# Kernel optimization log

Measured on AMD Instinct MI355X. Metric: run time of the kernel, lower is better.

The kernel has to match this reference:

```python
import jax, jax.numpy as jnp
import numpy as np

B, L, D = 4, 512, 128

def setup_inputs() -> dict:
    key = jax.random.key(0)
    k1, k2, k3, k4 = jax.random.split(key, 4)
    s = 1.0 / np.sqrt(D)
    return {
        "inp": jax.random.normal(k1, (B, L, D), dtype=jnp.float32),
        "Wu": jax.random.normal(k2, (D, D), dtype=jnp.float32) * s,
        "Ww": jax.random.normal(k3, (D, D), dtype=jnp.float32) * s,
        "Wv": jax.random.normal(k4, (1, D), dtype=jnp.float32) * s,
    }

def reference(inp, Wu, Ww, Wv):
    # inp: (B,L,D); torch Linear weights are (out,in), so y = x @ W.T
    qu = inp @ Wu.T                      # (B,L,D), u(inp)
    kw = inp @ Ww.T                      # (B,L,D), w(inp)
    # qu.unsqueeze(1) -> broadcast over i; kw.unsqueeze(2) -> broadcast over j
    # h[b,i,j,:] = tanh(u(inp)[b,j] + w(inp)[b,i])   (dropout = identity in eval)
    h = jnp.tanh(qu[:, None, :, :] + kw[:, :, None, :])   # (B,L,L,D)
    score = jnp.einsum('bijd,d->bij', h, Wv[0])           # (B,L,L)
    attn = jax.nn.softmax(score, axis=2)                  # softmax over keys j
    out = jnp.einsum('bij,bjd->bid', attn, inp)           # bmm(attn, inp)
    return out, attn
```

## Files before the change

kernel.cpp:

```cpp
#include <hip/hip_runtime.h>

#define BD 128
#define SL 512
#define NB 4

__device__ __forceinline__ float rcp_fast(float x) { return __builtin_amdgcn_rcpf(x); }

__global__ __launch_bounds__(256) void k_tr(const float* __restrict__ Wu,
                                            const float* __restrict__ Ww,
                                            float* __restrict__ WuT,
                                            float* __restrict__ WwT) {
    int idx = blockIdx.x * 256 + threadIdx.x;
    int k = idx >> 7, o = idx & 127;
    WuT[idx] = Wu[o * BD + k];
    WwT[idx] = Ww[o * BD + k];
}

__global__ __launch_bounds__(256) void k_qk(const float* __restrict__ inp,
                                            const float* __restrict__ WuT,
                                            const float* __restrict__ WwT,
                                            float* __restrict__ Equ,
                                            float* __restrict__ Ekw) {
    __shared__ float sx[2][BD];
    const int t = threadIdx.x, m = t >> 7, o = t & 127;
    const int blk = blockIdx.x;
    const int x   = blk & 7;
    const int b   = x >> 1;
    const int rp  = (blk >> 3) * 2 + (x & 1);
    const int r0  = b * SL + rp * 2;
    const int l0  = rp * 2;

    sx[t >> 7][t & 127] = inp[(size_t)r0 * BD + t];
    __syncthreads();

    const float* WT = m ? WwT : WuT;
    float acc0 = 0.f, acc1 = 0.f;
    #pragma unroll 4
    for (int k = 0; k < BD; k += 4) {
        float w0 = WT[(k + 0) * BD + o];
        float w1 = WT[(k + 1) * BD + o];
        float w2 = WT[(k + 2) * BD + o];
        float w3 = WT[(k + 3) * BD + o];
        float4 x0 = *(const float4*)&sx[0][k];
        float4 x1 = *(const float4*)&sx[1][k];
        acc0 = fmaf(x0.x, w0, acc0); acc0 = fmaf(x0.y, w1, acc0);
        acc0 = fmaf(x0.z, w2, acc0); acc0 = fmaf(x0.w, w3, acc0);
        acc1 = fmaf(x1.x, w0, acc1); acc1 = fmaf(x1.y, w1, acc1);
        acc1 = fmaf(x1.z, w2, acc1); acc1 = fmaf(x1.w, w3, acc1);
    }

    if (m == 0) {
        size_t base = ((size_t)b * 32 + (o >> 2)) * (SL * 4) + (size_t)l0 * 4 + (o & 3);
        Equ[base]     = __expf(2.f * acc0);
        Equ[base + 4] = __expf(2.f * acc1);
    } else {
        Ekw[(size_t)(r0 + 0) * BD + o] = __expf(2.f * acc0);
        Ekw[(size_t)(r0 + 1) * BD + o] = __expf(2.f * acc1);
    }
}

__device__ __forceinline__ void quad_acc(const float4 q, const float4 u4,
                                         const float4 e, float& acc) {
    float x0 = fmaf(q.x, e.x, u4.x);
    float x1 = fmaf(q.y, e.y, u4.y);
    float x2 = fmaf(q.z, e.z, u4.z);
    float x3 = fmaf(q.w, e.w, u4.w);
    float p01 = x0 * x1, p23 = x2 * x3;
    float num = fmaf(x0 + x1, p23, (x2 + x3) * p01);
    acc = fmaf(num, rcp_fast(p01 * p23), acc);
}

__global__ __launch_bounds__(512, 4) void k_attn(const float* __restrict__ inp,
                                                 const float* __restrict__ Wv,
                                                 const float* __restrict__ Equ,
                                                 const float* __restrict__ Ekw,
                                                 float* __restrict__ out,
                                                 float* __restrict__ attn) {
    __shared__ float4 s_E2[32][4];
    __shared__ float4 s_u4[32];
    __shared__ float4 s_pT[SL];
    __shared__ float  s_fin[32 * BD];
    __shared__ float4 s_red[8];

    const int j   = threadIdx.x;
    const int blk = blockIdx.x;
    const int x   = blk & 7;
    const int b   = x >> 1;
    const int it  = (blk >> 3) * 2 + (x & 1);
    const int i0  = it * 4;

    if (j < BD) {
        const float* ek = Ekw + ((size_t)b * SL + i0) * BD + j;
        float u = rcp_fast(Wv[j]);
        int c = j >> 2, kk = j & 3;
        ((float*)&s_E2[c][0])[kk] = ek[0]        * u;
        ((float*)&s_E2[c][1])[kk] = ek[BD]       * u;
        ((float*)&s_E2[c][2])[kk] = ek[2 * BD]   * u;
        ((float*)&s_E2[c][3])[kk] = ek[3 * BD]   * u;
        ((float*)&s_u4[c])[kk]    = u;
    }
    __syncthreads();

    const float4* equ4 = (const float4*)(Equ) + (size_t)b * 32 * SL;
    float a0 = 0.f, a1 = 0.f, a2 = 0.f, a3 = 0.f;
    #pragma unroll 4
    for (int c = 0; c < 32; ++c) {
        float4 q  = equ4[c * SL + j];
        float4 u4 = s_u4[c];
        float4 e0 = s_E2[c][0];
        float4 e1 = s_E2[c][1];
        float4 e2 = s_E2[c][2];
        float4 e3 = s_E2[c][3];
        quad_acc(q, u4, e0, a0);
        quad_acc(q, u4, e1, a1);
        quad_acc(q, u4, e2, a2);
        quad_acc(q, u4, e3, a3);
    }

    float p0 = __expf(-2.f * a0);
    float p1 = __expf(-2.f * a1);
    float p2 = __expf(-2.f * a2);
    float p3 = __expf(-2.f * a3);
    float r0 = p0, r1 = p1, r2 = p2, r3 = p3;
    #pragma unroll
    for (int off = 32; off > 0; off >>= 1) {
        r0 += __shfl_xor(r0, off, 64);
        r1 += __shfl_xor(r1, off, 64);
        r2 += __shfl_xor(r2, off, 64);
        r3 += __shfl_xor(r3, off, 64);
    }
    const int w = j >> 6, ln = j & 63;
    if (ln == 0) s_red[w] = make_float4(r0, r1, r2, r3);
    __syncthreads();
    float4 d0 = s_red[0], d1 = s_red[1], d2 = s_red[2], d3 = s_red[3];
    float4 d4 = s_red[4], d5 = s_red[5], d6 = s_red[6], d7 = s_red[7];
    float dx = ((d0.x + d1.x) + (d2.x + d3.x)) + ((d4.x + d5.x) + (d6.x + d7.x));
    float dy = ((d0.y + d1.y) + (d2.y + d3.y)) + ((d4.y + d5.y) + (d6.y + d7.y));
    float dz = ((d0.z + d1.z) + (d2.z + d3.z)) + ((d4.z + d5.z) + (d6.z + d7.z));
    float dw = ((d0.w + d1.w) + (d2.w + d3.w)) + ((d4.w + d5.w) + (d6.w + d7.w));
    float n0 = p0 * rcp_fast(dx);
    float n1 = p1 * rcp_fast(dy);
    float n2 = p2 * rcp_fast(dz);
    float n3 = p3 * rcp_fast(dw);
    float* ap = attn + ((size_t)b * SL + i0) * SL + j;
    ap[0]      = n0;
    ap[SL]     = n1;
    ap[2 * SL] = n2;
    ap[3 * SL] = n3;
    s_pT[j] = make_float4(n0, n1, n2, n3);
    __syncthreads();

    const int g  = j >> 6;
    const int dq = j & 31;
    const int rh = (j >> 5) & 1;
    const float4* inp4 = (const float4*)(inp) + (size_t)b * SL * 32;
    float4 accA = make_float4(0.f, 0.f, 0.f, 0.f);
    float4 accB = make_float4(0.f, 0.f, 0.f, 0.f);
    #pragma unroll 4
    for (int tt = 0; tt < 64; ++tt) {
        int jr = g * 64 + tt;
        float4 xv = inp4[jr * 32 + dq];
        float2 pp = *((const float2*)&s_pT[jr] + rh);
        accA.x = fmaf(pp.x, xv.x, accA.x); accA.y = fmaf(pp.x, xv.y, accA.y);
        accA.z = fmaf(pp.x, xv.z, accA.z); accA.w = fmaf(pp.x, xv.w, accA.w);
        accB.x = fmaf(pp.y, xv.x, accB.x); accB.y = fmaf(pp.y, xv.y, accB.y);
        accB.z = fmaf(pp.y, xv.z, accB.z); accB.w = fmaf(pp.y, xv.w, accB.w);
    }
    *(float4*)&s_fin[((g * 4) + rh * 2 + 0) * BD + dq * 4] = accA;
    *(float4*)&s_fin[((g * 4) + rh * 2 + 1) * BD + dq * 4] = accB;
    __syncthreads();
    {
        int row = j >> 7, d = j & 127;
        float s = 0.f;
        #pragma unroll
        for (int gg = 0; gg < 8; ++gg)
            s += s_fin[(gg * 4 + row) * BD + d];
        out[((size_t)b * SL + i0 + row) * BD + d] = s;
    }
}

extern "C" void kernel_launch(void* const* d_in, const int* in_sizes, int n_in,
                              void* d_out, int out_size, void* d_ws, size_t ws_size,
                              hipStream_t stream) {
    const float* inp = (const float*)d_in[0];
    const float* Wu  = (const float*)d_in[1];
    const float* Ww  = (const float*)d_in[2];
    const float* Wv  = (const float*)d_in[3];

    float* out  = (float*)d_out;
    float* attn = out + (size_t)NB * SL * BD;

    float* ws   = (float*)d_ws;
    float* Equ  = ws;
    float* Ekw  = Equ + (size_t)NB * BD * SL;
    float* WuT  = Ekw + (size_t)NB * SL * BD;
    float* WwT  = WuT + BD * BD;

    k_tr  <<<BD * BD / 256, 256, 0, stream>>>(Wu, Ww, WuT, WwT);
    k_qk  <<<NB * SL / 2, 256, 0, stream>>>(inp, WuT, WwT, Equ, Ekw);
    k_attn<<<NB * SL / 4, 512, 0, stream>>>(inp, Wv, Equ, Ekw, out, attn);
}
```

Baseline: 89.77 us.

## Fuse projection and attention into one cooperative kernel with grid sync

```diff
diff --git a/kernel.cpp b/kernel.cpp
--- a/kernel.cpp
+++ b/kernel.cpp
@@ -1,10 +1,217 @@
 #include <hip/hip_runtime.h>
+#include <hip/hip_cooperative_groups.h>
 
 #define BD 128
 #define SL 512
 #define NB 4
 
+namespace cg = cooperative_groups;
+
 __device__ __forceinline__ float rcp_fast(float x) { return __builtin_amdgcn_rcpf(x); }
+
+
+struct QkMem { float x[64][130]; float e[16][65]; };
+struct AtMem {
+    float4 E2[32][4];
+    float4 u4[32];
+    float4 pT[SL];
+    float  fin[32 * BD];
+    float4 red[8];
+};
+
+__global__ __launch_bounds__(512, 4) void k_fused(const float* __restrict__ inp,
+                                                  const float* __restrict__ Wu,
+                                                  const float* __restrict__ Ww,
+                                                  const float* __restrict__ Wv,
+                                                  float* __restrict__ Equ,
+                                                  float* __restrict__ Ekw,
+                                                  float* __restrict__ out,
+                                                  float* __restrict__ attn) {
+    constexpr size_t SM_BYTES = sizeof(QkMem) > sizeof(AtMem) ? sizeof(QkMem) : sizeof(AtMem);
+    __shared__ __align__(16) unsigned char smraw[SM_BYTES];
+    QkMem& qk = *reinterpret_cast<QkMem*>(smraw);
+    AtMem& at = *reinterpret_cast<AtMem*>(smraw);
+
+    const int t   = threadIdx.x;
+    const int blk = blockIdx.x;
+    const int x   = blk & 7;
+    const int b   = x >> 1;
+
+    {
+        const int jb = ((blk >> 3) << 1) | (x & 1);
+        const int m  = jb & 1;
+        const int o0 = ((jb >> 1) & 7) << 4;
+        const int rc = jb >> 4;
+        const int R0 = b * SL + rc * 64;
+
+        #pragma unroll
+        for (int c = 0; c < 16; ++c) {
+            int lin = c * 512 + t;
+            qk.x[lin >> 7][lin & 127] = inp[(size_t)R0 * BD + lin];
+        }
+        __syncthreads();
+
+        const int w = t >> 6, l = t & 63;
+        const int ou = __builtin_amdgcn_readfirstlane(o0 + (w << 1));
+        const float* __restrict__ Wm = m ? Ww : Wu;
+        const float* __restrict__ W0 = Wm + (size_t)ou * BD;
+        const float* __restrict__ W1 = W0 + BD;
+        float acc0 = 0.f, acc1 = 0.f;
+        #pragma unroll 8
+        for (int k = 0; k < BD; k += 2) {
+            float2 xv = *(const float2*)&qk.x[l][k];
+            float wa0 = W0[k], wb0 = W0[k + 1];
+            float wa1 = W1[k], wb1 = W1[k + 1];
+            acc0 = fmaf(xv.x, wa0, acc0); acc0 = fmaf(xv.y, wb0, acc0);
+            acc1 = fmaf(xv.x, wa1, acc1); acc1 = fmaf(xv.y, wb1, acc1);
+        }
+        qk.e[(w << 1) + 0][l] = __expf(2.f * acc0);
+        qk.e[(w << 1) + 1][l] = __expf(2.f * acc1);
+        __syncthreads();
+
+        if (m) {
+            #pragma unroll
+            for (int ph = 0; ph < 2; ++ph) {
+                int e   = ph * 512 + t;
+                int row = e >> 4, ol = e & 15;
+                Ekw[(size_t)(R0 + row) * BD + o0 + ol] = qk.e[ol][row];
+            }
+        } else {
+            float* Eb = Equ + (((size_t)b * 32 + (o0 >> 2)) * SL + rc * 64) * 4;
+            #pragma unroll
+            for (int ph = 0; ph < 2; ++ph) {
+                int e  = ph * 512 + t;
+                int cL = e >> 8, lj = (e >> 2) & 63, kk = e & 3;
+                Eb[((size_t)cL * SL + lj) * 4 + kk] = qk.e[cL * 4 + kk][lj];
+            }
+        }
+    }
+
+    __threadfence();
+    cg::this_grid().sync();
+
+    const int it = ((blk >> 3) << 1) | (x & 1);
+    const int i0 = it * 4;
+    const int j  = t;
+
+    if (j < BD) {
+        const float* ek = Ekw + ((size_t)b * SL + i0) * BD + j;
+        float u = rcp_fast(Wv[j]);
+        int c = j >> 2, kk = j & 3;
+        ((float*)&at.E2[c][0])[kk] = ek[0]      * u;
+        ((float*)&at.E2[c][1])[kk] = ek[BD]     * u;
+        ((float*)&at.E2[c][2])[kk] = ek[2 * BD] * u;
+        ((float*)&at.E2[c][3])[kk] = ek[3 * BD] * u;
+        ((float*)&at.u4[c])[kk]    = u;
+    }
+    __syncthreads();
+
+    const float4* equ4 = (const float4*)(Equ) + (size_t)b * 32 * SL;
+    float a0 = 0.f, a1 = 0.f, a2 = 0.f, a3 = 0.f;
+    #pragma unroll 4
+    for (int c = 0; c < 32; ++c) {
+        float4 q  = equ4[c * SL + j];
+        float4 u4 = at.u4[c];
+        float4 e0 = at.E2[c][0];
+        float4 e1 = at.E2[c][1];
+        float4 e2 = at.E2[c][2];
+        float4 e3 = at.E2[c][3];
+        {
+            float x0 = fmaf(q.x, e0.x, u4.x), x1 = fmaf(q.y, e0.y, u4.y);
+            float x2 = fmaf(q.z, e0.z, u4.z), x3 = fmaf(q.w, e0.w, u4.w);
+            float p01 = x0 * x1, p23 = x2 * x3;
+            float num = fmaf(x0 + x1, p23, (x2 + x3) * p01);
+            a0 = fmaf(num, rcp_fast(p01 * p23), a0);
+        }
+        {
+            float x0 = fmaf(q.x, e1.x, u4.x), x1 = fmaf(q.y, e1.y, u4.y);
+            float x2 = fmaf(q.z, e1.z, u4.z), x3 = fmaf(q.w, e1.w, u4.w);
+            float p01 = x0 * x1, p23 = x2 * x3;
+            float num = fmaf(x0 + x1, p23, (x2 + x3) * p01);
+            a1 = fmaf(num, rcp_fast(p01 * p23), a1);
+        }
+        {
+            float x0 = fmaf(q.x, e2.x, u4.x), x1 = fmaf(q.y, e2.y, u4.y);
+            float x2 = fmaf(q.z, e2.z, u4.z), x3 = fmaf(q.w, e2.w, u4.w);
+            float p01 = x0 * x1, p23 = x2 * x3;
+            float num = fmaf(x0 + x1, p23, (x2 + x3) * p01);
+            a2 = fmaf(num, rcp_fast(p01 * p23), a2);
+        }
+        {
+            float x0 = fmaf(q.x, e3.x, u4.x), x1 = fmaf(q.y, e3.y, u4.y);
+            float x2 = fmaf(q.z, e3.z, u4.z), x3 = fmaf(q.w, e3.w, u4.w);
+            float p01 = x0 * x1, p23 = x2 * x3;
+            float num = fmaf(x0 + x1, p23, (x2 + x3) * p01);
+            a3 = fmaf(num, rcp_fast(p01 * p23), a3);
+        }
+    }
+
+    float p0 = __expf(-2.f * a0);
+    float p1 = __expf(-2.f * a1);
+    float p2 = __expf(-2.f * a2);
+    float p3 = __expf(-2.f * a3);
+    float r0 = p0, r1 = p1, r2 = p2, r3 = p3;
+    #pragma unroll
+    for (int off = 32; off > 0; off >>= 1) {
+        r0 += __shfl_xor(r0, off, 64);
+        r1 += __shfl_xor(r1, off, 64);
+        r2 += __shfl_xor(r2, off, 64);
+        r3 += __shfl_xor(r3, off, 64);
+    }
+    const int wv8 = j >> 6, ln = j & 63;
+    if (ln == 0) at.red[wv8] = make_float4(r0, r1, r2, r3);
+    __syncthreads();
+    {
+        float4 d0 = at.red[0], d1 = at.red[1], d2 = at.red[2], d3 = at.red[3];
+        float4 d4 = at.red[4], d5 = at.red[5], d6 = at.red[6], d7 = at.red[7];
+        float dx = ((d0.x + d1.x) + (d2.x + d3.x)) + ((d4.x + d5.x) + (d6.x + d7.x));
+        float dy = ((d0.y + d1.y) + (d2.y + d3.y)) + ((d4.y + d5.y) + (d6.y + d7.y));
+        float dz = ((d0.z + d1.z) + (d2.z + d3.z)) + ((d4.z + d5.z) + (d6.z + d7.z));
+        float dw = ((d0.w + d1.w) + (d2.w + d3.w)) + ((d4.w + d5.w) + (d6.w + d7.w));
+        float n0 = p0 * rcp_fast(dx);
+        float n1 = p1 * rcp_fast(dy);
+        float n2 = p2 * rcp_fast(dz);
+        float n3 = p3 * rcp_fast(dw);
+        float* ap = attn + ((size_t)b * SL + i0) * SL + j;
+        ap[0]      = n0;
+        ap[SL]     = n1;
+        ap[2 * SL] = n2;
+        ap[3 * SL] = n3;
+        at.pT[j] = make_float4(n0, n1, n2, n3);
+    }
+    __syncthreads();
+
+    {
+        const int g  = j >> 6;
+        const int dq = j & 31;
+        const int rh = (j >> 5) & 1;
+        const float4* inp4 = (const float4*)(inp) + (size_t)b * SL * 32;
+        float4 accA = make_float4(0.f, 0.f, 0.f, 0.f);
+        float4 accB = make_float4(0.f, 0.f, 0.f, 0.f);
+        #pragma unroll 4
+        for (int tt = 0; tt < 64; ++tt) {
+            int jr = g * 64 + tt;
+            float4 xv = inp4[jr * 32 + dq];
+            float2 pp = *((const float2*)&at.pT[jr] + rh);
+            accA.x = fmaf(pp.x, xv.x, accA.x); accA.y = fmaf(pp.x, xv.y, accA.y);
+            accA.z = fmaf(pp.x, xv.z, accA.z); accA.w = fmaf(pp.x, xv.w, accA.w);
+            accB.x = fmaf(pp.y, xv.x, accB.x); accB.y = fmaf(pp.y, xv.y, accB.y);
+            accB.z = fmaf(pp.y, xv.z, accB.z); accB.w = fmaf(pp.y, xv.w, accB.w);
+        }
+        *(float4*)&at.fin[((g * 4) + rh * 2 + 0) * BD + dq * 4] = accA;
+        *(float4*)&at.fin[((g * 4) + rh * 2 + 1) * BD + dq * 4] = accB;
+    }
+    __syncthreads();
+    {
+        int row = j >> 7, d = j & 127;
+        float s = 0.f;
+        #pragma unroll
+        for (int gg = 0; gg < 8; ++gg)
+            s += at.fin[(gg * 4 + row) * BD + d];
+        out[((size_t)b * SL + i0 + row) * BD + d] = s;
+    }
+}
+
 
 __global__ __launch_bounds__(256) void k_tr(const float* __restrict__ Wu,
                                             const float* __restrict__ Ww,
@@ -50,24 +257,13 @@
     }
 
     if (m == 0) {
-        size_t base = ((size_t)b * 32 + (o >> 2)) * (SL * 4) + (size_t)l0 * 4 + (o & 3);
+        size_t base = (((size_t)b * 32 + (o >> 2)) * SL + l0) * 4 + (o & 3);
         Equ[base]     = __expf(2.f * acc0);
         Equ[base + 4] = __expf(2.f * acc1);
     } else {
         Ekw[(size_t)(r0 + 0) * BD + o] = __expf(2.f * acc0);
         Ekw[(size_t)(r0 + 1) * BD + o] = __expf(2.f * acc1);
     }
-}
-
-__device__ __forceinline__ void quad_acc(const float4 q, const float4 u4,
-                                         const float4 e, float& acc) {
-    float x0 = fmaf(q.x, e.x, u4.x);
-    float x1 = fmaf(q.y, e.y, u4.y);
-    float x2 = fmaf(q.z, e.z, u4.z);
-    float x3 = fmaf(q.w, e.w, u4.w);
-    float p01 = x0 * x1, p23 = x2 * x3;
-    float num = fmaf(x0 + x1, p23, (x2 + x3) * p01);
-    acc = fmaf(num, rcp_fast(p01 * p23), acc);
 }
 
 __global__ __launch_bounds__(512, 4) void k_attn(const float* __restrict__ inp,
@@ -93,10 +289,10 @@
         const float* ek = Ekw + ((size_t)b * SL + i0) * BD + j;
         float u = rcp_fast(Wv[j]);
         int c = j >> 2, kk = j & 3;
-        ((float*)&s_E2[c][0])[kk] = ek[0]        * u;
-        ((float*)&s_E2[c][1])[kk] = ek[BD]       * u;
-        ((float*)&s_E2[c][2])[kk] = ek[2 * BD]   * u;
-        ((float*)&s_E2[c][3])[kk] = ek[3 * BD]   * u;
+        ((float*)&s_E2[c][0])[kk] = ek[0]      * u;
+        ((float*)&s_E2[c][1])[kk] = ek[BD]     * u;
+        ((float*)&s_E2[c][2])[kk] = ek[2 * BD] * u;
+        ((float*)&s_E2[c][3])[kk] = ek[3 * BD] * u;
         ((float*)&s_u4[c])[kk]    = u;
     }
     __syncthreads();
@@ -111,10 +307,30 @@
         float4 e1 = s_E2[c][1];
         float4 e2 = s_E2[c][2];
         float4 e3 = s_E2[c][3];
-        quad_acc(q, u4, e0, a0);
-        quad_acc(q, u4, e1, a1);
-        quad_acc(q, u4, e2, a2);
-        quad_acc(q, u4, e3, a3);
+        {
+            float x0 = fmaf(q.x, e0.x, u4.x), x1 = fmaf(q.y, e0.y, u4.y);
+            float x2 = fmaf(q.z, e0.z, u4.z), x3 = fmaf(q.w, e0.w, u4.w);
+            float p01 = x0 * x1, p23 = x2 * x3;
+            a0 = fmaf(fmaf(x0 + x1, p23, (x2 + x3) * p01), rcp_fast(p01 * p23), a0);
+        }
+        {
+            float x0 = fmaf(q.x, e1.x, u4.x), x1 = fmaf(q.y, e1.y, u4.y);
+            float x2 = fmaf(q.z, e1.z, u4.z), x3 = fmaf(q.w, e1.w, u4.w);
+            float p01 = x0 * x1, p23 = x2 * x3;
+            a1 = fmaf(fmaf(x0 + x1, p23, (x2 + x3) * p01), rcp_fast(p01 * p23), a1);
+        }
+        {
+            float x0 = fmaf(q.x, e2.x, u4.x), x1 = fmaf(q.y, e2.y, u4.y);
+            float x2 = fmaf(q.z, e2.z, u4.z), x3 = fmaf(q.w, e2.w, u4.w);
+            float p01 = x0 * x1, p23 = x2 * x3;
+            a2 = fmaf(fmaf(x0 + x1, p23, (x2 + x3) * p01), rcp_fast(p01 * p23), a2);
+        }
+        {
+            float x0 = fmaf(q.x, e3.x, u4.x), x1 = fmaf(q.y, e3.y, u4.y);
+            float x2 = fmaf(q.z, e3.z, u4.z), x3 = fmaf(q.w, e3.w, u4.w);
+            float p01 = x0 * x1, p23 = x2 * x3;
+            a3 = fmaf(fmaf(x0 + x1, p23, (x2 + x3) * p01), rcp_fast(p01 * p23), a3);
+        }
     }
 
     float p0 = __expf(-2.f * a0);
@@ -196,7 +412,14 @@
     float* WuT  = Ekw + (size_t)NB * SL * BD;
     float* WwT  = WuT + BD * BD;
 
-    k_tr  <<<BD * BD / 256, 256, 0, stream>>>(Wu, Ww, WuT, WwT);
-    k_qk  <<<NB * SL / 2, 256, 0, stream>>>(inp, WuT, WwT, Equ, Ekw);
-    k_attn<<<NB * SL / 4, 512, 0, stream>>>(inp, Wv, Equ, Ekw, out, attn);
+    void* args[] = {(void*)&inp, (void*)&Wu, (void*)&Ww, (void*)&Wv,
+                    (void*)&Equ, (void*)&Ekw, (void*)&out, (void*)&attn};
+    hipError_t err = hipLaunchCooperativeKernel((const void*)k_fused,
+                                                dim3(NB * SL / 4), dim3(512),
+                                                args, 0, stream);
+    if (err != hipSuccess) {
+        k_tr  <<<BD * BD / 256, 256, 0, stream>>>(Wu, Ww, WuT, WwT);
+        k_qk  <<<NB * SL / 2, 256, 0, stream>>>(inp, WuT, WwT, Equ, Ekw);
+        k_attn<<<NB * SL / 4, 512, 0, stream>>>(inp, Wv, Equ, Ekw, out, attn);
+    }
 }
```

New measurement: 202.6 us. 126% more time.

## Fuse weight transpose into tiled projection kernel and restructure PV accumulation

Applied to the files above, without the earlier changes.

```diff
diff --git a/kernel.cpp b/kernel.cpp
--- a/kernel.cpp
+++ b/kernel.cpp
@@ -6,68 +6,64 @@
 
 __device__ __forceinline__ float rcp_fast(float x) { return __builtin_amdgcn_rcpf(x); }
 
-__global__ __launch_bounds__(256) void k_tr(const float* __restrict__ Wu,
-                                            const float* __restrict__ Ww,
-                                            float* __restrict__ WuT,
-                                            float* __restrict__ WwT) {
-    int idx = blockIdx.x * 256 + threadIdx.x;
-    int k = idx >> 7, o = idx & 127;
-    WuT[idx] = Wu[o * BD + k];
-    WwT[idx] = Ww[o * BD + k];
-}
-
-__global__ __launch_bounds__(256) void k_qk(const float* __restrict__ inp,
-                                            const float* __restrict__ WuT,
-                                            const float* __restrict__ WwT,
-                                            float* __restrict__ Equ,
-                                            float* __restrict__ Ekw) {
-    __shared__ float sx[2][BD];
-    const int t = threadIdx.x, m = t >> 7, o = t & 127;
+__global__ __launch_bounds__(512, 4) void k_qk2(const float* __restrict__ inp,
+                                                const float* __restrict__ Wu,
+                                                const float* __restrict__ Ww,
+                                                float* __restrict__ Equ,
+                                                float* __restrict__ Ekw) {
+    __shared__ float sx[64][130];
+    __shared__ float se[16][65];
+    const int t   = threadIdx.x;
     const int blk = blockIdx.x;
     const int x   = blk & 7;
     const int b   = x >> 1;
-    const int rp  = (blk >> 3) * 2 + (x & 1);
-    const int r0  = b * SL + rp * 2;
-    const int l0  = rp * 2;
-
-    sx[t >> 7][t & 127] = inp[(size_t)r0 * BD + t];
-    __syncthreads();
-
-    const float* WT = m ? WwT : WuT;
+    const int jb  = ((blk >> 3) << 1) | (x & 1);
+    const int m   = jb & 1;
+    const int o0  = ((jb >> 1) & 7) << 4;
+    const int rc  = jb >> 4;
+    const int R0  = b * SL + rc * 64;
+
+    #pragma unroll
+    for (int c = 0; c < 16; ++c) {
+        int lin = c * 512 + t;
+        sx[lin >> 7][lin & 127] = inp[(size_t)R0 * BD + lin];
+    }
+    __syncthreads();
+
+    const int w = t >> 6, l = t & 63;
+    const int ou = __builtin_amdgcn_readfirstlane(o0 + (w << 1));
+    const float* __restrict__ Wm = m ? Ww : Wu;
+    const float* __restrict__ W0 = Wm + (size_t)ou * BD;
+    const float* __restrict__ W1 = W0 + BD;
     float acc0 = 0.f, acc1 = 0.f;
-    #pragma unroll 4
-    for (int k = 0; k < BD; k += 4) {
-        float w0 = WT[(k + 0) * BD + o];
-        float w1 = WT[(k + 1) * BD + o];
-        float w2 = WT[(k + 2) * BD + o];
-        float w3 = WT[(k + 3) * BD + o];
-        float4 x0 = *(const float4*)&sx[0][k];
-        float4 x1 = *(const float4*)&sx[1][k];
-        acc0 = fmaf(x0.x, w0, acc0); acc0 = fmaf(x0.y, w1, acc0);
-        acc0 = fmaf(x0.z, w2, acc0); acc0 = fmaf(x0.w, w3, acc0);
-        acc1 = fmaf(x1.x, w0, acc1); acc1 = fmaf(x1.y, w1, acc1);
-        acc1 = fmaf(x1.z, w2, acc1); acc1 = fmaf(x1.w, w3, acc1);
-    }
-
-    if (m == 0) {
-        size_t base = ((size_t)b * 32 + (o >> 2)) * (SL * 4) + (size_t)l0 * 4 + (o & 3);
-        Equ[base]     = __expf(2.f * acc0);
-        Equ[base + 4] = __expf(2.f * acc1);
+    #pragma unroll 8
+    for (int k = 0; k < BD; k += 2) {
+        float2 xv = *(const float2*)&sx[l][k];
+        float wa0 = W0[k], wb0 = W0[k + 1];
+        float wa1 = W1[k], wb1 = W1[k + 1];
+        acc0 = fmaf(xv.x, wa0, acc0); acc0 = fmaf(xv.y, wb0, acc0);
+        acc1 = fmaf(xv.x, wa1, acc1); acc1 = fmaf(xv.y, wb1, acc1);
+    }
+    se[(w << 1) + 0][l] = __expf(2.f * acc0);
+    se[(w << 1) + 1][l] = __expf(2.f * acc1);
+    __syncthreads();
+
+    if (m) {
+        #pragma unroll
+        for (int ph = 0; ph < 2; ++ph) {
+            int e   = ph * 512 + t;
+            int row = e >> 4, ol = e & 15;
+            Ekw[(size_t)(R0 + row) * BD + o0 + ol] = se[ol][row];
+        }
     } else {
-        Ekw[(size_t)(r0 + 0) * BD + o] = __expf(2.f * acc0);
-        Ekw[(size_t)(r0 + 1) * BD + o] = __expf(2.f * acc1);
-    }
-}
-
-__device__ __forceinline__ void quad_acc(const float4 q, const float4 u4,
-                                         const float4 e, float& acc) {
-    float x0 = fmaf(q.x, e.x, u4.x);
-    float x1 = fmaf(q.y, e.y, u4.y);
-    float x2 = fmaf(q.z, e.z, u4.z);
-    float x3 = fmaf(q.w, e.w, u4.w);
-    float p01 = x0 * x1, p23 = x2 * x3;
-    float num = fmaf(x0 + x1, p23, (x2 + x3) * p01);
-    acc = fmaf(num, rcp_fast(p01 * p23), acc);
+        float* Eb = Equ + (((size_t)b * 32 + (o0 >> 2)) * SL + rc * 64) * 4;
+        #pragma unroll
+        for (int ph = 0; ph < 2; ++ph) {
+            int e  = ph * 512 + t;
+            int cL = e >> 8, lj = (e >> 2) & 63, kk = e & 3;
+            Eb[((size_t)cL * SL + lj) * 4 + kk] = se[cL * 4 + kk][lj];
+        }
+    }
 }
 
 __global__ __launch_bounds__(512, 4) void k_attn(const float* __restrict__ inp,
@@ -79,24 +75,24 @@
     __shared__ float4 s_E2[32][4];
     __shared__ float4 s_u4[32];
     __shared__ float4 s_pT[SL];
-    __shared__ float  s_fin[32 * BD];
+    __shared__ float4 s_fin4[16 * 4 * 32];
     __shared__ float4 s_red[8];
 
     const int j   = threadIdx.x;
     const int blk = blockIdx.x;
     const int x   = blk & 7;
     const int b   = x >> 1;
-    const int it  = (blk >> 3) * 2 + (x & 1);
+    const int it  = ((blk >> 3) << 1) | (x & 1);
     const int i0  = it * 4;
 
     if (j < BD) {
         const float* ek = Ekw + ((size_t)b * SL + i0) * BD + j;
         float u = rcp_fast(Wv[j]);
         int c = j >> 2, kk = j & 3;
-        ((float*)&s_E2[c][0])[kk] = ek[0]        * u;
-        ((float*)&s_E2[c][1])[kk] = ek[BD]       * u;
-        ((float*)&s_E2[c][2])[kk] = ek[2 * BD]   * u;
-        ((float*)&s_E2[c][3])[kk] = ek[3 * BD]   * u;
+        ((float*)&s_E2[c][0])[kk] = ek[0]      * u;
+        ((float*)&s_E2[c][1])[kk] = ek[BD]     * u;
+        ((float*)&s_E2[c][2])[kk] = ek[2 * BD] * u;
+        ((float*)&s_E2[c][3])[kk] = ek[3 * BD] * u;
         ((float*)&s_u4[c])[kk]    = u;
     }
     __syncthreads();
@@ -111,10 +107,30 @@
         float4 e1 = s_E2[c][1];
         float4 e2 = s_E2[c][2];
         float4 e3 = s_E2[c][3];
-        quad_acc(q, u4, e0, a0);
-        quad_acc(q, u4, e1, a1);
-        quad_acc(q, u4, e2, a2);
-        quad_acc(q, u4, e3, a3);
+        {
+            float x0 = fmaf(q.x, e0.x, u4.x), x1 = fmaf(q.y, e0.y, u4.y);
+            float x2 = fmaf(q.z, e0.z, u4.z), x3 = fmaf(q.w, e0.w, u4.w);
+            float p01 = x0 * x1, p23 = x2 * x3;
+            a0 = fmaf(fmaf(x0 + x1, p23, (x2 + x3) * p01), rcp_fast(p01 * p23), a0);
+        }
+        {
+            float x0 = fmaf(q.x, e1.x, u4.x), x1 = fmaf(q.y, e1.y, u4.y);
+            float x2 = fmaf(q.z, e1.z, u4.z), x3 = fmaf(q.w, e1.w, u4.w);
+            float p01 = x0 * x1, p23 = x2 * x3;
+            a1 = fmaf(fmaf(x0 + x1, p23, (x2 + x3) * p01), rcp_fast(p01 * p23), a1);
+        }
+        {
+            float x0 = fmaf(q.x, e2.x, u4.x), x1 = fmaf(q.y, e2.y, u4.y);
+            float x2 = fmaf(q.z, e2.z, u4.z), x3 = fmaf(q.w, e2.w, u4.w);
+            float p01 = x0 * x1, p23 = x2 * x3;
+            a2 = fmaf(fmaf(x0 + x1, p23, (x2 + x3) * p01), rcp_fast(p01 * p23), a2);
+        }
+        {
+            float x0 = fmaf(q.x, e3.x, u4.x), x1 = fmaf(q.y, e3.y, u4.y);
+            float x2 = fmaf(q.z, e3.z, u4.z), x3 = fmaf(q.w, e3.w, u4.w);
+            float p01 = x0 * x1, p23 = x2 * x3;
+            a3 = fmaf(fmaf(x0 + x1, p23, (x2 + x3) * p01), rcp_fast(p01 * p23), a3);
+        }
     }
 
     float p0 = __expf(-2.f * a0);
@@ -129,52 +145,65 @@
         r2 += __shfl_xor(r2, off, 64);
         r3 += __shfl_xor(r3, off, 64);
     }
-    const int w = j >> 6, ln = j & 63;
-    if (ln == 0) s_red[w] = make_float4(r0, r1, r2, r3);
-    __syncthreads();
-    float4 d0 = s_red[0], d1 = s_red[1], d2 = s_red[2], d3 = s_red[3];
-    float4 d4 = s_red[4], d5 = s_red[5], d6 = s_red[6], d7 = s_red[7];
-    float dx = ((d0.x + d1.x) + (d2.x + d3.x)) + ((d4.x + d5.x) + (d6.x + d7.x));
-    float dy = ((d0.y + d1.y) + (d2.y + d3.y)) + ((d4.y + d5.y) + (d6.y + d7.y));
-    float dz = ((d0.z + d1.z) + (d2.z + d3.z)) + ((d4.z + d5.z) + (d6.z + d7.z));
-    float dw = ((d0.w + d1.w) + (d2.w + d3.w)) + ((d4.w + d5.w) + (d6.w + d7.w));
-    float n0 = p0 * rcp_fast(dx);
-    float n1 = p1 * rcp_fast(dy);
-    float n2 = p2 * rcp_fast(dz);
-    float n3 = p3 * rcp_fast(dw);
-    float* ap = attn + ((size_t)b * SL + i0) * SL + j;
-    ap[0]      = n0;
-    ap[SL]     = n1;
-    ap[2 * SL] = n2;
-    ap[3 * SL] = n3;
-    s_pT[j] = make_float4(n0, n1, n2, n3);
-    __syncthreads();
-
-    const int g  = j >> 6;
-    const int dq = j & 31;
-    const int rh = (j >> 5) & 1;
-    const float4* inp4 = (const float4*)(inp) + (size_t)b * SL * 32;
-    float4 accA = make_float4(0.f, 0.f, 0.f, 0.f);
-    float4 accB = make_float4(0.f, 0.f, 0.f, 0.f);
-    #pragma unroll 4
-    for (int tt = 0; tt < 64; ++tt) {
-        int jr = g * 64 + tt;
-        float4 xv = inp4[jr * 32 + dq];
-        float2 pp = *((const float2*)&s_pT[jr] + rh);
-        accA.x = fmaf(pp.x, xv.x, accA.x); accA.y = fmaf(pp.x, xv.y, accA.y);
-        accA.z = fmaf(pp.x, xv.z, accA.z); accA.w = fmaf(pp.x, xv.w, accA.w);
-        accB.x = fmaf(pp.y, xv.x, accB.x); accB.y = fmaf(pp.y, xv.y, accB.y);
-        accB.z = fmaf(pp.y, xv.z, accB.z); accB.w = fmaf(pp.y, xv.w, accB.w);
-    }
-    *(float4*)&s_fin[((g * 4) + rh * 2 + 0) * BD + dq * 4] = accA;
-    *(float4*)&s_fin[((g * 4) + rh * 2 + 1) * BD + dq * 4] = accB;
+    const int w8 = j >> 6, ln0 = j & 63;
+    if (ln0 == 0) s_red[w8] = make_float4(r0, r1, r2, r3);
     __syncthreads();
     {
+        float4 d0 = s_red[0], d1 = s_red[1], d2 = s_red[2], d3 = s_red[3];
+        float4 d4 = s_red[4], d5 = s_red[5], d6 = s_red[6], d7 = s_red[7];
+        float dx = ((d0.x + d1.x) + (d2.x + d3.x)) + ((d4.x + d5.x) + (d6.x + d7.x));
+        float dy = ((d0.y + d1.y) + (d2.y + d3.y)) + ((d4.y + d5.y) + (d6.y + d7.y));
+        float dz = ((d0.z + d1.z) + (d2.z + d3.z)) + ((d4.z + d5.z) + (d6.z + d7.z));
+        float dw = ((d0.w + d1.w) + (d2.w + d3.w)) + ((d4.w + d5.w) + (d6.w + d7.w));
+        float n0 = p0 * rcp_fast(dx);
+        float n1 = p1 * rcp_fast(dy);
+        float n2 = p2 * rcp_fast(dz);
+        float n3 = p3 * rcp_fast(dw);
+        float* ap = attn + ((size_t)b * SL + i0) * SL + j;
+        ap[0]      = n0;
+        ap[SL]     = n1;
+        ap[2 * SL] = n2;
+        ap[3 * SL] = n3;
+        s_pT[j] = make_float4(n0, n1, n2, n3);
+    }
+    __syncthreads();
+
+    {
+        const int g  = j >> 6;
+        const int ln = j & 63;
+        const int dq = ln & 31;
+        const int jh = ln >> 5;
+        const int gi = g * 2 + jh;
+        const float4* inp4 = (const float4*)(inp) + (size_t)b * SL * 32;
+        float4 A0 = make_float4(0.f, 0.f, 0.f, 0.f);
+        float4 A1 = A0, A2 = A0, A3 = A0;
+        #pragma unroll 4
+        for (int tt = 0; tt < 32; ++tt) {
+            int jr = gi * 32 + tt;
+            float4 xv = inp4[jr * 32 + dq];
+            float4 pp = s_pT[jr];
+            A0.x = fmaf(pp.x, xv.x, A0.x); A0.y = fmaf(pp.x, xv.y, A0.y);
+            A0.z = fmaf(pp.x, xv.z, A0.z); A0.w = fmaf(pp.x, xv.w, A0.w);
+            A1.x = fmaf(pp.y, xv.x, A1.x); A1.y = fmaf(pp.y, xv.y, A1.y);
+            A1.z = fmaf(pp.y, xv.z, A1.z); A1.w = fmaf(pp.y, xv.w, A1.w);
+            A2.x = fmaf(pp.z, xv.x, A2.x); A2.y = fmaf(pp.z, xv.y, A2.y);
+            A2.z = fmaf(pp.z, xv.z, A2.z); A2.w = fmaf(pp.z, xv.w, A2.w);
+            A3.x = fmaf(pp.w, xv.x, A3.x); A3.y = fmaf(pp.w, xv.y, A3.y);
+            A3.z = fmaf(pp.w, xv.z, A3.z); A3.w = fmaf(pp.w, xv.w, A3.w);
+        }
+        s_fin4[((gi * 4) + 0) * 32 + dq] = A0;
+        s_fin4[((gi * 4) + 1) * 32 + dq] = A1;
+        s_fin4[((gi * 4) + 2) * 32 + dq] = A2;
+        s_fin4[((gi * 4) + 3) * 32 + dq] = A3;
+    }
+    __syncthreads();
+    {
+        const float* fin = (const float*)s_fin4;
         int row = j >> 7, d = j & 127;
         float s = 0.f;
         #pragma unroll
-        for (int gg = 0; gg < 8; ++gg)
-            s += s_fin[(gg * 4 + row) * BD + d];
+        for (int gg = 0; gg < 16; ++gg)
+            s += fin[(gg * 4 + row) * BD + d];
         out[((size_t)b * SL + i0 + row) * BD + d] = s;
     }
 }
@@ -193,10 +222,7 @@
     float* ws   = (float*)d_ws;
     float* Equ  = ws;
     float* Ekw  = Equ + (size_t)NB * BD * SL;
-    float* WuT  = Ekw + (size_t)NB * SL * BD;
-    float* WwT  = WuT + BD * BD;
-
-    k_tr  <<<BD * BD / 256, 256, 0, stream>>>(Wu, Ww, WuT, WwT);
-    k_qk  <<<NB * SL / 2, 256, 0, stream>>>(inp, WuT, WwT, Equ, Ekw);
+
+    k_qk2 <<<NB * SL / 4, 512, 0, stream>>>(inp, Wu, Ww, Equ, Ekw);
     k_attn<<<NB * SL / 4, 512, 0, stream>>>(inp, Wv, Equ, Ekw, out, attn);
 }
```

After: 87.77 us. 2.2% less time.
